# Performance work log

Hardware: AMD Instinct MI355X
Metric: run time of the kernel (lower is better)

## Reference

```python
import jax, jax.numpy as jnp
import numpy as np

T, B, D = 256, 64, 512


def setup_inputs() -> dict:
    key = jax.random.key(0)
    ks = jax.random.split(key, 9)
    s = 1.0 / np.sqrt(D)  # torch Linear default init scale (uniform), use scaled normal
    return {
        "x": jax.random.normal(ks[0], (T, B, D), dtype=jnp.float32),
        "y": jax.random.normal(ks[1], (T, B, D), dtype=jnp.float32),
        "Wr": jax.random.normal(ks[2], (D, D), dtype=jnp.float32) * s,
        "Ur": jax.random.normal(ks[3], (D, D), dtype=jnp.float32) * s,
        "Wz": jax.random.normal(ks[4], (D, D), dtype=jnp.float32) * s,
        "Uz": jax.random.normal(ks[5], (D, D), dtype=jnp.float32) * s,
        "Wg": jax.random.normal(ks[6], (D, D), dtype=jnp.float32) * s,
        "Ug": jax.random.normal(ks[7], (D, D), dtype=jnp.float32) * s,
        "bg": jnp.full((D,), 2.0, dtype=jnp.float32),
    }


def reference(x, y, Wr, Ur, Wz, Uz, Wg, Ug, bg):
    # GTrXL gating unit. torch Linear(y) == y @ W.T
    r = jax.nn.sigmoid(jnp.einsum("tbd,ed->tbe", y, Wr) + jnp.einsum("tbd,ed->tbe", x, Ur))
    z = jax.nn.sigmoid(jnp.einsum("tbd,ed->tbe", y, Wz) + jnp.einsum("tbd,ed->tbe", x, Uz) - bg)
    h = jnp.tanh(jnp.einsum("tbd,ed->tbe", y, Wg) + jnp.einsum("tbd,ed->tbe", r * x, Ug))
    g = (1.0 - z) * x + z * h  # (T, B, D)
    return g
```

## Files before the change

### kernel.cpp

```cpp
#include <hip/hip_runtime.h>
#include <stdint.h>

typedef unsigned short u16;
typedef unsigned long long u64;
typedef __attribute__((ext_vector_type(8))) __bf16 bf16x8;
typedef __attribute__((ext_vector_type(4))) float f32x4;

#define Dn 512
#define Mn 16384


__device__ __forceinline__ u16 f2bf(float f) {
  unsigned u = __float_as_uint(f);
  u += 0x7fffu + ((u >> 16) & 1u);
  return (u16)(u >> 16);
}

__device__ __forceinline__ float bf2f(u16 b) {
  return __uint_as_float(((unsigned)b) << 16);
}

__device__ __forceinline__ void async16(const u16* g, u16* l) {
  __builtin_amdgcn_global_load_lds(
      (const __attribute__((address_space(1))) unsigned int*)g,
      (__attribute__((address_space(3))) unsigned int*)l, 16, 0, 0);
}

__device__ __forceinline__ float sigmoidf_(float v) {
  return 1.f / (1.f + __expf(-v));
}

__device__ __forceinline__ void st_u64_coh(u64* p, u64 v) {
  __hip_atomic_store(p, v, __ATOMIC_RELAXED, __HIP_MEMORY_SCOPE_AGENT);
}
__device__ __forceinline__ void st_u16_coh(u16* p, u16 v) {
  __hip_atomic_store(p, v, __ATOMIC_RELAXED, __HIP_MEMORY_SCOPE_AGENT);
}

__device__ __forceinline__ u64 pack4bf(float4 v) {
  u64 r = (u64)f2bf(v.x) | ((u64)f2bf(v.y) << 16) |
          ((u64)f2bf(v.z) << 32) | ((u64)f2bf(v.w) << 48);
  return r;
}

__global__ void cast_w(const float* w0, const float* w1, const float* w2,
                       const float* w3, const float* w4, const float* w5,
                       u16* __restrict__ bRZ, u16* __restrict__ bG) {
  const int b = (int)blockIdx.x;
  const int t = (int)threadIdx.x;
  const int wi = b >> 8;
  const int bb = b & 255;
  const float* src = wi == 0 ? w0 : wi == 1 ? w1 : wi == 2 ? w2
                   : wi == 3 ? w3 : wi == 4 ? w4 : w5;
  const int i4 = bb * 256 + t;
  const int e  = i4 >> 7;
  const int c4 = i4 & 127;
  float4 v = ((const float4*)src)[i4];
  ushort4 o;
  o.x = f2bf(v.x); o.y = f2bf(v.y); o.z = f2bf(v.z); o.w = f2bf(v.w);
  ushort4* base = (wi >= 4) ? (ushort4*)bG : (ushort4*)bRZ;
  const int row = e + ((wi == 2 || wi == 3) ? 512 : 0);
  const int off = row * 256 + c4 + ((wi & 1) ? 128 : 0);
  base[off] = o;
}

struct GArgs {
  const float *yf, *xf, *bg;
  u16 *yb, *xb, *rxb, *zb;
  const u16 *bRZ, *bG;
  float* out;
  unsigned *cflag, *rflag;
};

__global__ __launch_bounds__(256, 4) void fused_rzgu(GArgs a) {
  __shared__ u16 smem[16384];
  const int tid = (int)threadIdx.x;
  const int lane = tid & 63;
  const int wave = tid >> 6;
  const int waveM = wave >> 1, waveN = wave & 1;
  const int wbyte = (tid & 192) * 16;
  const int lm = lane & 15, quad = lane >> 4;
  const int srow = tid >> 3;
  const int scol = (((tid & 7) ^ ((tid >> 3) & 7)) * 8);
  const int lswz = lm & 7;
  const int mb = (int)blockIdx.x & 127, nb = (int)blockIdx.x >> 7;
  const int rowStart = mb * 128, colStart = nb * 128;

  {
    const int r0 = rowStart + nb * 16;
#pragma unroll
    for (int k = tid; k < 2048; k += 256) {
      const int gi = (r0 + (k >> 7)) * 128 + (k & 127);
      st_u64_coh((u64*)a.yb + gi, pack4bf(((const float4*)a.yf)[gi]));
      st_u64_coh((u64*)a.xb + gi, pack4bf(((const float4*)a.xf)[gi]));
    }
  }
  asm volatile("s_waitcnt vmcnt(0)" ::: "memory");
  __syncthreads();
  if (tid == 0) {
    __hip_atomic_fetch_add(&a.cflag[mb], 1u, __ATOMIC_RELAXED, __HIP_MEMORY_SCOPE_AGENT);
    unsigned spins = 0;
    while (__hip_atomic_load(&a.cflag[mb], __ATOMIC_RELAXED, __HIP_MEMORY_SCOPE_AGENT) < 8u) {
      __builtin_amdgcn_s_sleep(4);
      if (++spins > (1u << 20)) break;
    }
  }
  __syncthreads();
  __builtin_amdgcn_sched_barrier(0);

  {
    u16* sA = smem;
    u16* sB = smem + 8192;

    f32x4 acc[4][4] = {};

    for (int kq = 0; kq < 16; ++kq) {
      const int half = kq >> 3;
      const int k0 = (kq & 7) * 64;
      const u16* abase = half ? a.xb : a.yb;
#pragma unroll
      for (int s = 0; s < 4; ++s) {
        async16(abase + (size_t)(rowStart + s * 32 + srow) * 512 + k0 + scol,
                (u16*)((char*)sA + s * 4096 + wbyte));
        async16(a.bRZ + (size_t)(colStart + s * 32 + srow) * 1024 + kq * 64 + scol,
                (u16*)((char*)sB + s * 4096 + wbyte));
      }
      __syncthreads();

#pragma unroll
      for (int kk = 0; kk < 2; ++kk) {
        bf16x8 aa[4], bw[4];
#pragma unroll
        for (int i = 0; i < 4; ++i)
          aa[i] = *(const bf16x8*)(sA + (waveM * 64 + i * 16 + lm) * 64 +
                                   ((kk * 4 + quad) ^ lswz) * 8);
#pragma unroll
        for (int j = 0; j < 4; ++j)
          bw[j] = *(const bf16x8*)(sB + (waveN * 64 + j * 16 + lm) * 64 +
                                   ((kk * 4 + quad) ^ lswz) * 8);
#pragma unroll
        for (int i = 0; i < 4; ++i)
#pragma unroll
          for (int j = 0; j < 4; ++j)
            acc[i][j] = __builtin_amdgcn_mfma_f32_16x16x32_bf16(aa[i], bw[j], acc[i][j], 0, 0, 0);
      }
      __syncthreads();
    }

    if (colStart < 512) {
#pragma unroll
      for (int j = 0; j < 4; ++j) {
        const int e = colStart + waveN * 64 + j * 16 + lm;
#pragma unroll
        for (int i = 0; i < 4; ++i) {
          const int m0 = rowStart + waveM * 64 + i * 16 + quad * 4;
#pragma unroll
          for (int rg = 0; rg < 4; ++rg) {
            const size_t idx = (size_t)(m0 + rg) * 512 + e;
            const float r = sigmoidf_(acc[i][j][rg]);
            st_u16_coh(&a.rxb[idx], f2bf(r * bf2f(a.xb[idx])));
          }
        }
      }
    } else {
#pragma unroll
      for (int j = 0; j < 4; ++j) {
        const int e = colStart - 512 + waveN * 64 + j * 16 + lm;
        const float bgv = a.bg[e];
#pragma unroll
        for (int i = 0; i < 4; ++i) {
          const int m0 = rowStart + waveM * 64 + i * 16 + quad * 4;
#pragma unroll
          for (int rg = 0; rg < 4; ++rg) {
            const size_t idx = (size_t)(m0 + rg) * 512 + e;
            st_u16_coh(&a.zb[idx], f2bf(sigmoidf_(acc[i][j][rg] - bgv)));
          }
        }
      }
    }
  }
  asm volatile("s_waitcnt vmcnt(0)" ::: "memory");
  __syncthreads();
  if (tid == 0)
    __hip_atomic_fetch_add(&a.rflag[mb], 1u, __ATOMIC_RELAXED, __HIP_MEMORY_SCOPE_AGENT);

  {
    u16* sA = smem;
    u16* sB = smem + 4096;
    const int rowG = rowStart + (nb & 1) * 64;
    const int colG = (nb >> 1) * 128;

    f32x4 acc[2][4] = {};

    for (int kq = 0; kq < 8; ++kq) {
      const int k0 = kq * 64;
#pragma unroll
      for (int s = 0; s < 2; ++s)
        async16(a.yb + (size_t)(rowG + s * 32 + srow) * 512 + k0 + scol,
                (u16*)((char*)sA + s * 4096 + wbyte));
#pragma unroll
      for (int s = 0; s < 4; ++s)
        async16(a.bG + (size_t)(colG + s * 32 + srow) * 1024 + kq * 64 + scol,
                (u16*)((char*)sB + s * 4096 + wbyte));
      __syncthreads();

#pragma unroll
      for (int kk = 0; kk < 2; ++kk) {
        bf16x8 aa[2], bw[4];
#pragma unroll
        for (int i = 0; i < 2; ++i)
          aa[i] = *(const bf16x8*)(sA + (waveM * 32 + i * 16 + lm) * 64 +
                                   ((kk * 4 + quad) ^ lswz) * 8);
#pragma unroll
        for (int j = 0; j < 4; ++j)
          bw[j] = *(const bf16x8*)(sB + (waveN * 64 + j * 16 + lm) * 64 +
                                   ((kk * 4 + quad) ^ lswz) * 8);
#pragma unroll
        for (int i = 0; i < 2; ++i)
#pragma unroll
          for (int j = 0; j < 4; ++j)
            acc[i][j] = __builtin_amdgcn_mfma_f32_16x16x32_bf16(aa[i], bw[j], acc[i][j], 0, 0, 0);
      }
      __syncthreads();
    }

    if (tid == 0) {
      unsigned spins = 0;
      while (__hip_atomic_load(&a.rflag[mb], __ATOMIC_RELAXED, __HIP_MEMORY_SCOPE_AGENT) < 8u) {
        __builtin_amdgcn_s_sleep(4);
        if (++spins > (1u << 20)) break;
      }
    }
    __syncthreads();
    __builtin_amdgcn_sched_barrier(0);

    for (int kq = 8; kq < 16; ++kq) {
      const int k0 = (kq & 7) * 64;
#pragma unroll
      for (int s = 0; s < 2; ++s)
        async16(a.rxb + (size_t)(rowG + s * 32 + srow) * 512 + k0 + scol,
                (u16*)((char*)sA + s * 4096 + wbyte));
#pragma unroll
      for (int s = 0; s < 4; ++s)
        async16(a.bG + (size_t)(colG + s * 32 + srow) * 1024 + kq * 64 + scol,
                (u16*)((char*)sB + s * 4096 + wbyte));
      __syncthreads();

#pragma unroll
      for (int kk = 0; kk < 2; ++kk) {
        bf16x8 aa[2], bw[4];
#pragma unroll
        for (int i = 0; i < 2; ++i)
          aa[i] = *(const bf16x8*)(sA + (waveM * 32 + i * 16 + lm) * 64 +
                                   ((kk * 4 + quad) ^ lswz) * 8);
#pragma unroll
        for (int j = 0; j < 4; ++j)
          bw[j] = *(const bf16x8*)(sB + (waveN * 64 + j * 16 + lm) * 64 +
                                   ((kk * 4 + quad) ^ lswz) * 8);
#pragma unroll
        for (int i = 0; i < 2; ++i)
#pragma unroll
          for (int j = 0; j < 4; ++j)
            acc[i][j] = __builtin_amdgcn_mfma_f32_16x16x32_bf16(aa[i], bw[j], acc[i][j], 0, 0, 0);
      }
      __syncthreads();
    }

#pragma unroll
    for (int j = 0; j < 4; ++j) {
      const int e = colG + waveN * 64 + j * 16 + lm;
#pragma unroll
      for (int i = 0; i < 2; ++i) {
        const int m0 = rowG + waveM * 32 + i * 16 + quad * 4;
#pragma unroll
        for (int rg = 0; rg < 4; ++rg) {
          const size_t idx = (size_t)(m0 + rg) * 512 + e;
          const float pre = acc[i][j][rg];
          const float ex = __expf(-2.f * pre);
          const float h = (1.f - ex) / (1.f + ex);
          const float z = bf2f(a.zb[idx]);
          const float xv = bf2f(a.xb[idx]);
          a.out[idx] = (1.f - z) * xv + z * h;
        }
      }
    }
  }
}

extern "C" void kernel_launch(void* const* d_in, const int* in_sizes, int n_in,
                              void* d_out, int out_size, void* d_ws, size_t ws_size,
                              hipStream_t stream) {
  const float* x  = (const float*)d_in[0];
  const float* y  = (const float*)d_in[1];
  const float* Wr = (const float*)d_in[2];
  const float* Ur = (const float*)d_in[3];
  const float* Wz = (const float*)d_in[4];
  const float* Uz = (const float*)d_in[5];
  const float* Wg = (const float*)d_in[6];
  const float* Ug = (const float*)d_in[7];
  const float* bg = (const float*)d_in[8];

  char* ws = (char*)d_ws;
  u16* yb  = (u16*)(ws);
  u16* xb  = (u16*)(ws + 16777216);
  u16* rxb = (u16*)(ws + 2 * 16777216);
  u16* zb  = (u16*)(ws + 3 * 16777216);
  u16* bRZ = (u16*)(ws + 4 * 16777216);
  u16* bG  = (u16*)(ws + 4 * 16777216 + 2097152);
  char* flags = ws + 4 * 16777216 + 2097152 + 1048576;

  GArgs ga;
  ga.yf = y; ga.xf = x; ga.bg = bg;
  ga.yb = yb; ga.xb = xb; ga.rxb = rxb; ga.zb = zb;
  ga.bRZ = bRZ; ga.bG = bG;
  ga.out = (float*)d_out;
  ga.cflag = (unsigned*)flags;
  ga.rflag = (unsigned*)(flags + 512);

  hipMemsetAsync(flags, 0, 1024, stream);
  cast_w<<<1536, 256, 0, stream>>>(Wr, Ur, Wz, Uz, Wg, Ug, bRZ, bG);
  fused_rzgu<<<1024, 256, 0, stream>>>(ga);
}
```

Before: 230.2 us.

## Fuse weight bf16 cast into main kernel with global completion counter

Removes the separate cast_w launch: the first 128 blocks of the fused kernel each convert a slice of the six weight matrices to bf16, then bump a global counter, and every block spins until all 128 have finished before starting the GEMMs. The block index mapping also changes so each group of 8 consecutive blocks shares one row block (mb = b>>3). This saves a kernel launch and its inter-kernel gap. In exchange it adds a grid-wide spin barrier that relies on the first 128 blocks being resident, plus extra work on those blocks.

```diff
diff --git a/kernel.cpp b/kernel.cpp
--- a/kernel.cpp
+++ b/kernel.cpp
@@ -43,33 +43,12 @@
   return r;
 }
 
-__global__ void cast_w(const float* w0, const float* w1, const float* w2,
-                       const float* w3, const float* w4, const float* w5,
-                       u16* __restrict__ bRZ, u16* __restrict__ bG) {
-  const int b = (int)blockIdx.x;
-  const int t = (int)threadIdx.x;
-  const int wi = b >> 8;
-  const int bb = b & 255;
-  const float* src = wi == 0 ? w0 : wi == 1 ? w1 : wi == 2 ? w2
-                   : wi == 3 ? w3 : wi == 4 ? w4 : w5;
-  const int i4 = bb * 256 + t;
-  const int e  = i4 >> 7;
-  const int c4 = i4 & 127;
-  float4 v = ((const float4*)src)[i4];
-  ushort4 o;
-  o.x = f2bf(v.x); o.y = f2bf(v.y); o.z = f2bf(v.z); o.w = f2bf(v.w);
-  ushort4* base = (wi >= 4) ? (ushort4*)bG : (ushort4*)bRZ;
-  const int row = e + ((wi == 2 || wi == 3) ? 512 : 0);
-  const int off = row * 256 + c4 + ((wi & 1) ? 128 : 0);
-  base[off] = o;
-}
-
 struct GArgs {
   const float *yf, *xf, *bg;
-  u16 *yb, *xb, *rxb, *zb;
-  const u16 *bRZ, *bG;
+  const float *w0, *w1, *w2, *w3, *w4, *w5;
+  u16 *yb, *xb, *rxb, *zb, *bRZ, *bG;
   float* out;
-  unsigned *cflag, *rflag;
+  unsigned *cflag, *rflag, *wcnt;
 };
 
 __global__ __launch_bounds__(256, 4) void fused_rzgu(GArgs a) {
@@ -83,8 +62,26 @@
   const int srow = tid >> 3;
   const int scol = (((tid & 7) ^ ((tid >> 3) & 7)) * 8);
   const int lswz = lm & 7;
-  const int mb = (int)blockIdx.x & 127, nb = (int)blockIdx.x >> 7;
+  const int b = (int)blockIdx.x;
+  const int mb = b >> 3, nb = b & 7;
   const int rowStart = mb * 128, colStart = nb * 128;
+
+  if (b < 128) {
+#pragma unroll
+    for (int i = 0; i < 12; ++i) {
+      const int g = (b * 256 + tid) + i * 32768;
+      const int wi = g >> 16;
+      const int i4 = g & 65535;
+      const float* src = wi == 0 ? a.w0 : wi == 1 ? a.w1 : wi == 2 ? a.w2
+                       : wi == 3 ? a.w3 : wi == 4 ? a.w4 : a.w5;
+      const int e  = i4 >> 7;
+      const int c4 = i4 & 127;
+      const int row = e + ((wi == 2 || wi == 3) ? 512 : 0);
+      const int off = row * 256 + c4 + ((wi & 1) ? 128 : 0);
+      u64* base = (wi >= 4) ? (u64*)a.bG : (u64*)a.bRZ;
+      st_u64_coh(base + off, pack4bf(((const float4*)src)[i4]));
+    }
+  }
 
   {
     const int r0 = rowStart + nb * 16;
@@ -98,8 +95,15 @@
   asm volatile("s_waitcnt vmcnt(0)" ::: "memory");
   __syncthreads();
   if (tid == 0) {
+    if (b < 128)
+      __hip_atomic_fetch_add(a.wcnt, 1u, __ATOMIC_RELAXED, __HIP_MEMORY_SCOPE_AGENT);
     __hip_atomic_fetch_add(&a.cflag[mb], 1u, __ATOMIC_RELAXED, __HIP_MEMORY_SCOPE_AGENT);
     unsigned spins = 0;
+    while (__hip_atomic_load(a.wcnt, __ATOMIC_RELAXED, __HIP_MEMORY_SCOPE_AGENT) < 128u) {
+      __builtin_amdgcn_s_sleep(4);
+      if (++spins > (1u << 20)) break;
+    }
+    spins = 0;
     while (__hip_atomic_load(&a.cflag[mb], __ATOMIC_RELAXED, __HIP_MEMORY_SCOPE_AGENT) < 8u) {
       __builtin_amdgcn_s_sleep(4);
       if (++spins > (1u << 20)) break;
@@ -290,16 +294,6 @@
 extern "C" void kernel_launch(void* const* d_in, const int* in_sizes, int n_in,
                               void* d_out, int out_size, void* d_ws, size_t ws_size,
                               hipStream_t stream) {
-  const float* x  = (const float*)d_in[0];
-  const float* y  = (const float*)d_in[1];
-  const float* Wr = (const float*)d_in[2];
-  const float* Ur = (const float*)d_in[3];
-  const float* Wz = (const float*)d_in[4];
-  const float* Uz = (const float*)d_in[5];
-  const float* Wg = (const float*)d_in[6];
-  const float* Ug = (const float*)d_in[7];
-  const float* bg = (const float*)d_in[8];
-
   char* ws = (char*)d_ws;
   u16* yb  = (u16*)(ws);
   u16* xb  = (u16*)(ws + 16777216);
@@ -310,14 +304,22 @@
   char* flags = ws + 4 * 16777216 + 2097152 + 1048576;
 
   GArgs ga;
-  ga.yf = y; ga.xf = x; ga.bg = bg;
+  ga.yf = (const float*)d_in[1];
+  ga.xf = (const float*)d_in[0];
+  ga.bg = (const float*)d_in[8];
+  ga.w0 = (const float*)d_in[2];
+  ga.w1 = (const float*)d_in[3];
+  ga.w2 = (const float*)d_in[4];
+  ga.w3 = (const float*)d_in[5];
+  ga.w4 = (const float*)d_in[6];
+  ga.w5 = (const float*)d_in[7];
   ga.yb = yb; ga.xb = xb; ga.rxb = rxb; ga.zb = zb;
   ga.bRZ = bRZ; ga.bG = bG;
   ga.out = (float*)d_out;
   ga.cflag = (unsigned*)flags;
   ga.rflag = (unsigned*)(flags + 512);
-
-  hipMemsetAsync(flags, 0, 1024, stream);
-  cast_w<<<1536, 256, 0, stream>>>(Wr, Ur, Wz, Uz, Wg, Ug, bRZ, bG);
+  ga.wcnt  = (unsigned*)(flags + 1024);
+
+  hipMemsetAsync(flags, 0, 2048, stream);
   fused_rzgu<<<1024, 256, 0, stream>>>(ga);
 }
```

Result: no change. 230.5 us (+0.1%).
